# Optimization experiments

Measured on AMD Instinct MI355X. Metric: run time of the kernel, lower is better.

Reference implementation:

```python
import jax, jax.numpy as jnp
import numpy as np

HEADS = 8
DIM_HEAD = 64
SCALE = DIM_HEAD ** -0.5


def setup_inputs() -> dict:
    key = jax.random.key(0)
    ks = jax.random.split(key, 8)
    B, Nq, Nk, D = 4, 1024, 2048, 512
    inner = HEADS * DIM_HEAD  # 512
    x = jax.random.normal(ks[0], (B, Nq, D), dtype=jnp.float32)
    context = jax.random.normal(ks[1], (B, Nk, D), dtype=jnp.float32)
    bias = jax.random.normal(ks[2], (B, Nq, Nk), dtype=jnp.float32)
    s = D ** -0.5
    Wq = jax.random.normal(ks[3], (inner, D), dtype=jnp.float32) * s
    Wk = jax.random.normal(ks[4], (inner, D), dtype=jnp.float32) * s
    Wv = jax.random.normal(ks[5], (inner, D), dtype=jnp.float32) * s
    Wo = jax.random.normal(ks[6], (D, inner), dtype=jnp.float32) * s
    bo = jnp.zeros((D,), dtype=jnp.float32)
    return {"x": x, "context": context, "bias": bias,
            "Wq": Wq, "Wk": Wk, "Wv": Wv, "Wo": Wo, "bo": bo}


def reference(x, context, bias, Wq, Wk, Wv, Wo, bo):
    B, Nq, _ = x.shape
    # torch Linear: y = x @ W.T ; reshape (h d) -> b h n d
    q = (x @ Wq.T).reshape(B, Nq, HEADS, DIM_HEAD).transpose(0, 2, 1, 3)
    k = (context @ Wk.T).reshape(B, -1, HEADS, DIM_HEAD).transpose(0, 2, 1, 3)
    v = (context @ Wv.T).reshape(B, -1, HEADS, DIM_HEAD).transpose(0, 2, 1, 3)
    # explicit-score fallback path (bias supplied)
    scores = jnp.einsum('bhqd,bhkd->bhqk', q, k) * SCALE
    scores = scores + bias[:, None, :, :]  # 3D bias -> (B,1,Nq,Nk)
    attn = jax.nn.softmax(scores, axis=-1)
    out = jnp.einsum('bhqk,bhkd->bhqd', attn, v)
    out = out.transpose(0, 2, 1, 3).reshape(B, Nq, HEADS * DIM_HEAD)
    return out @ Wo.T + bo
```

## Files before the change

kernel.cpp:

```cpp
#include <hip/hip_runtime.h>

#define H 8
#define DH 64
#define NQ 1024
#define NK 2048
#define DIN 512
#define B 4
#define KSPLIT 2
#define KRANGE (NK / KSPLIT)
#define KTILES (KRANGE / 64)
#define BHNQ (B * H * NQ)

typedef __bf16 bf16;
typedef __bf16 bf16x8 __attribute__((ext_vector_type(8)));
typedef __bf16 bf16x4 __attribute__((ext_vector_type(4)));
typedef float floatx4 __attribute__((ext_vector_type(4)));

__device__ inline void gload16(const void* g, void* l) {
  __builtin_amdgcn_global_load_lds(
      (const __attribute__((address_space(1))) void*)g,
      (__attribute__((address_space(3))) void*)l, 16, 0, 0);
}

__global__ void cvt_all(const float* __restrict__ x, const float* __restrict__ ctx,
                        const float* __restrict__ wq, const float* __restrict__ wk,
                        const float* __restrict__ wv, const float* __restrict__ wo,
                        bf16* xb, bf16* cb, bf16* wqb, bf16* wkb, bf16* wvb, bf16* wob) {
  long i = ((long)blockIdx.x * 256 + threadIdx.x) * 4;
  const float* s; bf16* d; long o;
  if (i < 2097152)      { s = x;   d = xb;  o = i; }
  else if (i < 6291456) { s = ctx; d = cb;  o = i - 2097152; }
  else if (i < 6553600) { s = wq;  d = wqb; o = i - 6291456; }
  else if (i < 6815744) { s = wk;  d = wkb; o = i - 6553600; }
  else if (i < 7077888) { s = wv;  d = wvb; o = i - 6815744; }
  else                  { s = wo;  d = wob; o = i - 7077888; }
  float4 f = *(const float4*)(s + o);
  bf16x4 v = { (bf16)f.x, (bf16)f.y, (bf16)f.z, (bf16)f.w };
  *(bf16x4*)(d + o) = v;
}

__global__ __launch_bounds__(256) void gemm_qkv(
    const bf16* __restrict__ xb, const bf16* __restrict__ cb,
    const bf16* __restrict__ wqb, const bf16* __restrict__ wkb, const bf16* __restrict__ wvb,
    bf16* __restrict__ qb, bf16* __restrict__ kb, bf16* __restrict__ vtb) {
  const int which = blockIdx.z;
  if (which == 0 && blockIdx.y >= 64) return;
  const bf16* A = (which == 0) ? xb : cb;
  const bf16* W = (which == 0) ? wqb : ((which == 1) ? wkb : wvb);
  bf16* outb = (which == 0) ? qb : ((which == 1) ? kb : vtb);
  const int logT = (which == 0) ? 10 : 11;
  const float scale = (which == 0) ? 0.125f : 1.0f;
  const bool vmode = (which == 2);

  __shared__ bf16 Al[2][64 * 32];
  __shared__ bf16 Bl[2][128 * 32];
  const int t = threadIdx.x;
  const int lane = t & 63, w = t >> 6;
  const int ln = lane & 15, quad = lane >> 4;
  const int wm = (w >> 1) * 32, wn = (w & 1) * 64;
  const int rowBase = blockIdx.y * 64;
  const int colBase = blockIdx.x * 128;

  floatx4 acc[2][4] = {};
  const int rA = t >> 2, oA = (t & 3) * 8;
  const int c0 = t, c1 = t + 256;
  const int rB0 = c0 >> 2, oB0 = (c0 & 3) * 8;
  const int rB1 = c1 >> 2, oB1 = (c1 & 3) * 8;
  const bf16* Ab = A + (size_t)rowBase * DIN;
  const bf16* Wb = W + (size_t)colBase * DIN;

  gload16(Ab + (size_t)rA * DIN + oA, &Al[0][t * 8]);
  gload16(Wb + (size_t)rB0 * DIN + oB0, &Bl[0][c0 * 8]);
  gload16(Wb + (size_t)rB1 * DIN + oB1, &Bl[0][c1 * 8]);
  __syncthreads();

  for (int k0 = 0; k0 < DIN; k0 += 32) {
    const int cur = (k0 >> 5) & 1, nxt = cur ^ 1;
    if (k0 + 32 < DIN) {
      gload16(Ab + (size_t)rA * DIN + k0 + 32 + oA, &Al[nxt][t * 8]);
      gload16(Wb + (size_t)rB0 * DIN + k0 + 32 + oB0, &Bl[nxt][c0 * 8]);
      gload16(Wb + (size_t)rB1 * DIN + k0 + 32 + oB1, &Bl[nxt][c1 * 8]);
    }
    bf16x8 af[2], bfr[4];
#pragma unroll
    for (int i = 0; i < 2; i++)
      af[i] = *(const bf16x8*)&Al[cur][(wm + i * 16 + ln) * 32 + quad * 8];
#pragma unroll
    for (int j = 0; j < 4; j++)
      bfr[j] = *(const bf16x8*)&Bl[cur][(wn + j * 16 + ln) * 32 + quad * 8];
    if (!vmode) {
#pragma unroll
      for (int i = 0; i < 2; i++)
#pragma unroll
        for (int j = 0; j < 4; j++)
          acc[i][j] = __builtin_amdgcn_mfma_f32_16x16x32_bf16(af[i], bfr[j], acc[i][j], 0, 0, 0);
    } else {
#pragma unroll
      for (int i = 0; i < 2; i++)
#pragma unroll
        for (int j = 0; j < 4; j++)
          acc[i][j] = __builtin_amdgcn_mfma_f32_16x16x32_bf16(bfr[j], af[i], acc[i][j], 0, 0, 0);
    }
    __syncthreads();
  }

  const int T = 1 << logT;
#pragma unroll
  for (int i = 0; i < 2; i++)
#pragma unroll
    for (int j = 0; j < 4; j++)
#pragma unroll
      for (int r = 0; r < 4; r++) {
        if (!vmode) {
          const int m = rowBase + wm + i * 16 + quad * 4 + r;
          const int n = colBase + wn + j * 16 + ln;
          const float v = acc[i][j][r] * scale;
          const int bb = m >> logT, tok = m & (T - 1);
          const int hh = n >> 6, d = n & 63;
          outb[((((size_t)(bb * H + hh)) << logT) + tok) * DH + d] = (bf16)v;
        } else {
          const int dg = colBase + wn + j * 16 + quad * 4 + r;
          const int m = rowBase + wm + i * 16 + ln;
          const int bb = m >> logT, tok = m & (T - 1);
          const int hh = dg >> 6, d = dg & 63;
          outb[(((size_t)(bb * H + hh) * DH + d) << logT) + tok] = (bf16)acc[i][j][r];
        }
      }
}

__global__ __launch_bounds__(128) void attn_fwd(
    const bf16* __restrict__ q, const bf16* __restrict__ k,
    const bf16* __restrict__ vt, const float* __restrict__ bias,
    float* __restrict__ op0, float* __restrict__ op1, float* __restrict__ lpart) {
  __shared__ bf16 KL[64 * 64];
  __shared__ bf16 VL[64 * 64];
  __shared__ bf16 Pl[2][2][16 * 64];
  const int tid = threadIdx.x;
  const int lane = tid & 63, w = tid >> 6;
  const int ln = lane & 15, quad = lane >> 4;
  const int hh = blockIdx.y;
  const int b = blockIdx.z >> 1, ks = blockIdx.z & 1;
  const int q0 = blockIdx.x * 64;
  const int k0 = ks * KRANGE;
  const size_t bh = (size_t)b * H + hh;
  const bf16* qp = q + bh * NQ * DH;
  const bf16* kp = k + bh * NK * DH;
  const bf16* vp = vt + bh * DH * NK;
  const float* bp = bias + ((size_t)b * NQ + q0 + w * 32 + quad * 4) * NK + ln;

  bf16x8 qf[2][2];
#pragma unroll
  for (int s = 0; s < 2; s++)
#pragma unroll
    for (int kc = 0; kc < 2; kc++)
      qf[s][kc] = *(const bf16x8*)(qp + (size_t)(q0 + w * 32 + s * 16 + ln) * DH + kc * 32 + quad * 8);

  floatx4 o[2][4] = {};
  floatx4 lac[2] = {};
  const bf16x8 ones = {(bf16)1.f, (bf16)1.f, (bf16)1.f, (bf16)1.f,
                       (bf16)1.f, (bf16)1.f, (bf16)1.f, (bf16)1.f};
  constexpr float L2E = 1.44269504f;
  constexpr float OFF = 34.6246810f;

  for (int tt = 0; tt < KTILES; tt++) {
    const int nk0 = k0 + tt * 64;
#pragma unroll
    for (int s = 0; s < 4; s++) {
      const int i = s * 128 + tid;
      const int sr = i >> 3, sc = (i & 7) ^ (sr & 7);
      gload16(kp + (size_t)(nk0 + sr) * DH + sc * 8, &KL[i * 8]);
      gload16(vp + (size_t)sr * NK + nk0 + sc * 8, &VL[i * 8]);
    }
    float bc[2][4][4];
#pragma unroll
    for (int s = 0; s < 2; s++)
#pragma unroll
      for (int j = 0; j < 4; j++)
#pragma unroll
        for (int r = 0; r < 4; r++)
          bc[s][j][r] = bp[(size_t)(s * 16 + r) * NK + nk0 + j * 16];
    __syncthreads();

    floatx4 s4[2][4];
#pragma unroll
    for (int s = 0; s < 2; s++)
#pragma unroll
      for (int j = 0; j < 4; j++) {
        s4[s][j][0] = bc[s][j][0]; s4[s][j][1] = bc[s][j][1];
        s4[s][j][2] = bc[s][j][2]; s4[s][j][3] = bc[s][j][3];
      }
#pragma unroll
    for (int j = 0; j < 4; j++)
#pragma unroll
      for (int kc = 0; kc < 2; kc++) {
        const int kr = j * 16 + ln;
        bf16x8 kf = *(const bf16x8*)&KL[kr * 64 + (((kc * 4 + quad) ^ (kr & 7)) * 8)];
        s4[0][j] = __builtin_amdgcn_mfma_f32_16x16x32_bf16(qf[0][kc], kf, s4[0][j], 0, 0, 0);
        s4[1][j] = __builtin_amdgcn_mfma_f32_16x16x32_bf16(qf[1][kc], kf, s4[1][j], 0, 0, 0);
      }

#pragma unroll
    for (int s = 0; s < 2; s++)
#pragma unroll
      for (int j = 0; j < 4; j++)
#pragma unroll
        for (int r = 0; r < 4; r++)
          s4[s][j][r] = exp2f(fmaf(s4[s][j][r], L2E, -OFF));

#pragma unroll
    for (int s = 0; s < 2; s++)
#pragma unroll
      for (int j = 0; j < 4; j++)
#pragma unroll
        for (int r = 0; r < 4; r++) {
          const int m = quad * 4 + r;
          Pl[w][s][m * 64 + (((j * 2 + (ln >> 3)) ^ (m & 7)) * 8) + (ln & 7)] = (bf16)s4[s][j][r];
        }
    asm volatile("s_waitcnt lgkmcnt(0)" ::: "memory");
    bf16x8 pf[2][2];
#pragma unroll
    for (int s = 0; s < 2; s++)
#pragma unroll
      for (int kc = 0; kc < 2; kc++)
        pf[s][kc] = *(const bf16x8*)&Pl[w][s][ln * 64 + (((kc * 4 + quad) ^ (ln & 7)) * 8)];

#pragma unroll
    for (int s = 0; s < 2; s++)
#pragma unroll
      for (int kc = 0; kc < 2; kc++)
        lac[s] = __builtin_amdgcn_mfma_f32_16x16x32_bf16(pf[s][kc], ones, lac[s], 0, 0, 0);

#pragma unroll
    for (int jn = 0; jn < 4; jn++)
#pragma unroll
      for (int kc = 0; kc < 2; kc++) {
        const int vr = jn * 16 + ln;
        bf16x8 vf = *(const bf16x8*)&VL[vr * 64 + (((kc * 4 + quad) ^ (vr & 7)) * 8)];
        o[0][jn] = __builtin_amdgcn_mfma_f32_16x16x32_bf16(pf[0][kc], vf, o[0][jn], 0, 0, 0);
        o[1][jn] = __builtin_amdgcn_mfma_f32_16x16x32_bf16(pf[1][kc], vf, o[1][jn], 0, 0, 0);
      }
    __syncthreads();
  }

#pragma unroll
  for (int s = 0; s < 2; s++) {
    float* op = (ks ? op1 : op0) +
                ((size_t)b * NQ + q0 + w * 32 + s * 16 + quad * 4) * DIN + hh * 64 + ln;
#pragma unroll
    for (int jn = 0; jn < 4; jn++)
#pragma unroll
      for (int r = 0; r < 4; r++)
        op[(size_t)r * DIN + jn * 16] = o[s][jn][r];
    if (ln == 0) {
      float4 lv = {lac[s][0], lac[s][1], lac[s][2], lac[s][3]};
      *(float4*)&lpart[((size_t)ks * B * H + b * H + hh) * NQ + q0 + w * 32 + s * 16 + quad * 4] = lv;
    }
  }
}

__global__ __launch_bounds__(256) void gemm_out(
    const float* __restrict__ op0, const float* __restrict__ op1,
    const float* __restrict__ lp, const bf16* __restrict__ W,
    float* __restrict__ outf, const float* __restrict__ bo) {
  __shared__ bf16 Al[2][64 * 32];
  __shared__ bf16 Bl[2][128 * 32];
  const int t = threadIdx.x;
  const int lane = t & 63, w = t >> 6;
  const int ln = lane & 15, quad = lane >> 4;
  const int wm = (w >> 1) * 32, wn = (w & 1) * 64;
  const int rowBase = blockIdx.y * 64;
  const int colBase = blockIdx.x * 128;

  floatx4 acc[2][4] = {};
  const int rA = t >> 2, oA = (t & 3) * 8;
  const int c0 = t, c1 = t + 256;
  const int rB0 = c0 >> 2, oB0 = (c0 & 3) * 8;
  const int rB1 = c1 >> 2, oB1 = (c1 & 3) * 8;
  const int m0 = rowBase + rA;
  const bf16* Wb = W + (size_t)colBase * DIN;

  float linv0[8];
#pragma unroll
  for (int h = 0; h < 8; h++) {
    const int i0 = ((m0 >> 10) * H + h) * NQ + (m0 & 1023);
    linv0[h] = 1.0f / (lp[i0] + lp[BHNQ + i0]);
  }

#define STAGE_A(K0V, BUF)                                                      \
  {                                                                            \
    const float sA = linv0[(K0V) >> 6];                                        \
    const float* pa0 = op0 + (size_t)m0 * DIN + (K0V) + oA;                    \
    const float* pa1 = op1 + (size_t)m0 * DIN + (K0V) + oA;                    \
    float4 xa = *(const float4*)pa0, xb2 = *(const float4*)(pa0 + 4);          \
    float4 ya = *(const float4*)pa1, yb = *(const float4*)(pa1 + 4);           \
    bf16x8 v0 = {(bf16)((xa.x + ya.x) * sA), (bf16)((xa.y + ya.y) * sA),       \
                 (bf16)((xa.z + ya.z) * sA), (bf16)((xa.w + ya.w) * sA),       \
                 (bf16)((xb2.x + yb.x) * sA), (bf16)((xb2.y + yb.y) * sA),     \
                 (bf16)((xb2.z + yb.z) * sA), (bf16)((xb2.w + yb.w) * sA)};    \
    *(bf16x8*)&Al[BUF][t * 8] = v0;                                            \
  }

  STAGE_A(0, 0);
  gload16(Wb + (size_t)rB0 * DIN + oB0, &Bl[0][c0 * 8]);
  gload16(Wb + (size_t)rB1 * DIN + oB1, &Bl[0][c1 * 8]);
  __syncthreads();

#pragma unroll
  for (int kk = 0; kk < 16; kk++) {
    const int cur = kk & 1, nxt = cur ^ 1;
    if (kk < 15) {
      const int k1 = (kk + 1) * 32;
      STAGE_A(k1, nxt);
      gload16(Wb + (size_t)rB0 * DIN + k1 + oB0, &Bl[nxt][c0 * 8]);
      gload16(Wb + (size_t)rB1 * DIN + k1 + oB1, &Bl[nxt][c1 * 8]);
    }
    bf16x8 af[2], bfr[4];
#pragma unroll
    for (int i = 0; i < 2; i++)
      af[i] = *(const bf16x8*)&Al[cur][(wm + i * 16 + ln) * 32 + quad * 8];
#pragma unroll
    for (int j = 0; j < 4; j++)
      bfr[j] = *(const bf16x8*)&Bl[cur][(wn + j * 16 + ln) * 32 + quad * 8];
#pragma unroll
    for (int i = 0; i < 2; i++)
#pragma unroll
      for (int j = 0; j < 4; j++)
        acc[i][j] = __builtin_amdgcn_mfma_f32_16x16x32_bf16(af[i], bfr[j], acc[i][j], 0, 0, 0);
    __syncthreads();
  }
#undef STAGE_A

#pragma unroll
  for (int i = 0; i < 2; i++)
#pragma unroll
    for (int j = 0; j < 4; j++)
#pragma unroll
      for (int r = 0; r < 4; r++) {
        const int m = rowBase + wm + i * 16 + quad * 4 + r;
        const int n = colBase + wn + j * 16 + ln;
        outf[(size_t)m * DIN + n] = acc[i][j][r] + bo[n];
      }
}

extern "C" void kernel_launch(void* const* d_in, const int* in_sizes, int n_in,
                              void* d_out, int out_size, void* d_ws, size_t ws_size,
                              hipStream_t stream) {
  const float* x    = (const float*)d_in[0];
  const float* ctx  = (const float*)d_in[1];
  const float* bias = (const float*)d_in[2];
  const float* Wq   = (const float*)d_in[3];
  const float* Wk   = (const float*)d_in[4];
  const float* Wv   = (const float*)d_in[5];
  const float* Wo   = (const float*)d_in[6];
  const float* bo   = (const float*)d_in[7];
  float* out = (float*)d_out;

  char* p = (char*)d_ws;
  bf16* xb   = (bf16*)(p + 0);
  bf16* cb   = (bf16*)(p + 4194304);
  bf16* wqb  = (bf16*)(p + 12582912);
  bf16* wkb  = (bf16*)(p + 13107200);
  bf16* wvb  = (bf16*)(p + 13631488);
  bf16* wob  = (bf16*)(p + 14155776);
  bf16* qb   = (bf16*)(p + 14680064);
  bf16* kb   = (bf16*)(p + 18874368);
  bf16* vtb  = (bf16*)(p + 27262976);
  float* op1 = (float*)(p + 35651584);
  float* lpart = (float*)(p + 44040192);
  float* op0 = (float*)cb;

  cvt_all<<<7168, 256, 0, stream>>>(x, ctx, Wq, Wk, Wv, Wo, xb, cb, wqb, wkb, wvb, wob);
  gemm_qkv<<<dim3(4, 128, 3), 256, 0, stream>>>(xb, cb, wqb, wkb, wvb, qb, kb, vtb);
  attn_fwd<<<dim3(NQ / 64, H, B * KSPLIT), 128, 0, stream>>>(qb, kb, vtb, bias, op0, op1, lpart);
  gemm_out<<<dim3(4, 64), 256, 0, stream>>>(op0, op1, lpart, wob, out, bo);
}
```

Measured before the change: 196.6 us.

## Pre-convert bias to bf16, fuse x/ctx conversion into QKV GEMM, bf16 partials

```diff
diff --git a/kernel.cpp b/kernel.cpp
--- a/kernel.cpp
+++ b/kernel.cpp
@@ -22,30 +22,29 @@
       (__attribute__((address_space(3))) void*)l, 16, 0, 0);
 }
 
-__global__ void cvt_all(const float* __restrict__ x, const float* __restrict__ ctx,
+__global__ void cvt_all(const float* __restrict__ bias,
                         const float* __restrict__ wq, const float* __restrict__ wk,
                         const float* __restrict__ wv, const float* __restrict__ wo,
-                        bf16* xb, bf16* cb, bf16* wqb, bf16* wkb, bf16* wvb, bf16* wob) {
+                        bf16* bias16, bf16* wqb, bf16* wkb, bf16* wvb, bf16* wob) {
   long i = ((long)blockIdx.x * 256 + threadIdx.x) * 4;
   const float* s; bf16* d; long o;
-  if (i < 2097152)      { s = x;   d = xb;  o = i; }
-  else if (i < 6291456) { s = ctx; d = cb;  o = i - 2097152; }
-  else if (i < 6553600) { s = wq;  d = wqb; o = i - 6291456; }
-  else if (i < 6815744) { s = wk;  d = wkb; o = i - 6553600; }
-  else if (i < 7077888) { s = wv;  d = wvb; o = i - 6815744; }
-  else                  { s = wo;  d = wob; o = i - 7077888; }
+  if (i < 8388608)      { s = bias; d = bias16; o = i; }
+  else if (i < 8650752) { s = wq;  d = wqb; o = i - 8388608; }
+  else if (i < 8912896) { s = wk;  d = wkb; o = i - 8650752; }
+  else if (i < 9175040) { s = wv;  d = wvb; o = i - 8912896; }
+  else                  { s = wo;  d = wob; o = i - 9175040; }
   float4 f = *(const float4*)(s + o);
   bf16x4 v = { (bf16)f.x, (bf16)f.y, (bf16)f.z, (bf16)f.w };
   *(bf16x4*)(d + o) = v;
 }
 
 __global__ __launch_bounds__(256) void gemm_qkv(
-    const bf16* __restrict__ xb, const bf16* __restrict__ cb,
+    const float* __restrict__ x, const float* __restrict__ ctx,
     const bf16* __restrict__ wqb, const bf16* __restrict__ wkb, const bf16* __restrict__ wvb,
     bf16* __restrict__ qb, bf16* __restrict__ kb, bf16* __restrict__ vtb) {
   const int which = blockIdx.z;
   if (which == 0 && blockIdx.y >= 64) return;
-  const bf16* A = (which == 0) ? xb : cb;
+  const float* A32 = (which == 0) ? x : ctx;
   const bf16* W = (which == 0) ? wqb : ((which == 1) ? wkb : wvb);
   bf16* outb = (which == 0) ? qb : ((which == 1) ? kb : vtb);
   const int logT = (which == 0) ? 10 : 11;
@@ -66,20 +65,29 @@
   const int c0 = t, c1 = t + 256;
   const int rB0 = c0 >> 2, oB0 = (c0 & 3) * 8;
   const int rB1 = c1 >> 2, oB1 = (c1 & 3) * 8;
-  const bf16* Ab = A + (size_t)rowBase * DIN;
+  const float* Ab = A32 + (size_t)(rowBase + rA) * DIN + oA;
   const bf16* Wb = W + (size_t)colBase * DIN;
 
-  gload16(Ab + (size_t)rA * DIN + oA, &Al[0][t * 8]);
+  float4 la0, la1;
+  la0 = *(const float4*)(Ab + 0);
+  la1 = *(const float4*)(Ab + 4);
+  {
+    bf16x8 v = {(bf16)la0.x, (bf16)la0.y, (bf16)la0.z, (bf16)la0.w,
+                (bf16)la1.x, (bf16)la1.y, (bf16)la1.z, (bf16)la1.w};
+    *(bf16x8*)&Al[0][t * 8] = v;
+  }
   gload16(Wb + (size_t)rB0 * DIN + oB0, &Bl[0][c0 * 8]);
   gload16(Wb + (size_t)rB1 * DIN + oB1, &Bl[0][c1 * 8]);
   __syncthreads();
 
-  for (int k0 = 0; k0 < DIN; k0 += 32) {
-    const int cur = (k0 >> 5) & 1, nxt = cur ^ 1;
-    if (k0 + 32 < DIN) {
-      gload16(Ab + (size_t)rA * DIN + k0 + 32 + oA, &Al[nxt][t * 8]);
-      gload16(Wb + (size_t)rB0 * DIN + k0 + 32 + oB0, &Bl[nxt][c0 * 8]);
-      gload16(Wb + (size_t)rB1 * DIN + k0 + 32 + oB1, &Bl[nxt][c1 * 8]);
+  for (int kk = 0; kk < 16; kk++) {
+    const int cur = kk & 1, nxt = cur ^ 1;
+    const int k1 = (kk + 1) * 32;
+    if (kk < 15) {
+      la0 = *(const float4*)(Ab + k1);
+      la1 = *(const float4*)(Ab + k1 + 4);
+      gload16(Wb + (size_t)rB0 * DIN + k1 + oB0, &Bl[nxt][c0 * 8]);
+      gload16(Wb + (size_t)rB1 * DIN + k1 + oB1, &Bl[nxt][c1 * 8]);
     }
     bf16x8 af[2], bfr[4];
 #pragma unroll
@@ -100,6 +108,11 @@
 #pragma unroll
         for (int j = 0; j < 4; j++)
           acc[i][j] = __builtin_amdgcn_mfma_f32_16x16x32_bf16(bfr[j], af[i], acc[i][j], 0, 0, 0);
+    }
+    if (kk < 15) {
+      bf16x8 v = {(bf16)la0.x, (bf16)la0.y, (bf16)la0.z, (bf16)la0.w,
+                  (bf16)la1.x, (bf16)la1.y, (bf16)la1.z, (bf16)la1.w};
+      *(bf16x8*)&Al[nxt][t * 8] = v;
     }
     __syncthreads();
   }
@@ -130,10 +143,11 @@
 
 __global__ __launch_bounds__(128) void attn_fwd(
     const bf16* __restrict__ q, const bf16* __restrict__ k,
-    const bf16* __restrict__ vt, const float* __restrict__ bias,
-    float* __restrict__ op0, float* __restrict__ op1, float* __restrict__ lpart) {
+    const bf16* __restrict__ vt, const bf16* __restrict__ bias16,
+    bf16* __restrict__ op0, bf16* __restrict__ op1, float* __restrict__ lpart) {
   __shared__ bf16 KL[64 * 64];
   __shared__ bf16 VL[64 * 64];
+  __shared__ bf16 BL[64 * 64];
   __shared__ bf16 Pl[2][2][16 * 64];
   const int tid = threadIdx.x;
   const int lane = tid & 63, w = tid >> 6;
@@ -146,7 +160,7 @@
   const bf16* qp = q + bh * NQ * DH;
   const bf16* kp = k + bh * NK * DH;
   const bf16* vp = vt + bh * DH * NK;
-  const float* bp = bias + ((size_t)b * NQ + q0 + w * 32 + quad * 4) * NK + ln;
+  const bf16* bb = bias16 + ((size_t)b * NQ + q0) * NK;
 
   bf16x8 qf[2][2];
 #pragma unroll
@@ -170,25 +184,11 @@
       const int sr = i >> 3, sc = (i & 7) ^ (sr & 7);
       gload16(kp + (size_t)(nk0 + sr) * DH + sc * 8, &KL[i * 8]);
       gload16(vp + (size_t)sr * NK + nk0 + sc * 8, &VL[i * 8]);
-    }
-    float bc[2][4][4];
-#pragma unroll
-    for (int s = 0; s < 2; s++)
-#pragma unroll
-      for (int j = 0; j < 4; j++)
-#pragma unroll
-        for (int r = 0; r < 4; r++)
-          bc[s][j][r] = bp[(size_t)(s * 16 + r) * NK + nk0 + j * 16];
+      gload16(bb + (size_t)sr * NK + nk0 + sc * 8, &BL[i * 8]);
+    }
     __syncthreads();
 
-    floatx4 s4[2][4];
-#pragma unroll
-    for (int s = 0; s < 2; s++)
-#pragma unroll
-      for (int j = 0; j < 4; j++) {
-        s4[s][j][0] = bc[s][j][0]; s4[s][j][1] = bc[s][j][1];
-        s4[s][j][2] = bc[s][j][2]; s4[s][j][3] = bc[s][j][3];
-      }
+    floatx4 s4[2][4] = {};
 #pragma unroll
     for (int j = 0; j < 4; j++)
 #pragma unroll
@@ -204,8 +204,11 @@
 #pragma unroll
       for (int j = 0; j < 4; j++)
 #pragma unroll
-        for (int r = 0; r < 4; r++)
-          s4[s][j][r] = exp2f(fmaf(s4[s][j][r], L2E, -OFF));
+        for (int r = 0; r < 4; r++) {
+          const int m = w * 32 + s * 16 + quad * 4 + r;
+          const float bv = (float)BL[m * 64 + (((j * 2 + (ln >> 3)) ^ (m & 7)) * 8) + (ln & 7)];
+          s4[s][j][r] = exp2f(fmaf(s4[s][j][r] + bv, L2E, -OFF));
+        }
 
 #pragma unroll
     for (int s = 0; s < 2; s++)
@@ -244,13 +247,13 @@
 
 #pragma unroll
   for (int s = 0; s < 2; s++) {
-    float* op = (ks ? op1 : op0) +
-                ((size_t)b * NQ + q0 + w * 32 + s * 16 + quad * 4) * DIN + hh * 64 + ln;
+    bf16* op = (ks ? op1 : op0) +
+               ((size_t)b * NQ + q0 + w * 32 + s * 16 + quad * 4) * DIN + hh * 64 + ln;
 #pragma unroll
     for (int jn = 0; jn < 4; jn++)
 #pragma unroll
       for (int r = 0; r < 4; r++)
-        op[(size_t)r * DIN + jn * 16] = o[s][jn][r];
+        op[(size_t)r * DIN + jn * 16] = (bf16)o[s][jn][r];
     if (ln == 0) {
       float4 lv = {lac[s][0], lac[s][1], lac[s][2], lac[s][3]};
       *(float4*)&lpart[((size_t)ks * B * H + b * H + hh) * NQ + q0 + w * 32 + s * 16 + quad * 4] = lv;
@@ -259,7 +262,7 @@
 }
 
 __global__ __launch_bounds__(256) void gemm_out(
-    const float* __restrict__ op0, const float* __restrict__ op1,
+    const bf16* __restrict__ op0, const bf16* __restrict__ op1,
     const float* __restrict__ lp, const bf16* __restrict__ W,
     float* __restrict__ outf, const float* __restrict__ bo) {
   __shared__ bf16 Al[2][64 * 32];
@@ -289,14 +292,12 @@
 #define STAGE_A(K0V, BUF)                                                      \
   {                                                                            \
     const float sA = linv0[(K0V) >> 6];                                        \
-    const float* pa0 = op0 + (size_t)m0 * DIN + (K0V) + oA;                    \
-    const float* pa1 = op1 + (size_t)m0 * DIN + (K0V) + oA;                    \
-    float4 xa = *(const float4*)pa0, xb2 = *(const float4*)(pa0 + 4);          \
-    float4 ya = *(const float4*)pa1, yb = *(const float4*)(pa1 + 4);           \
-    bf16x8 v0 = {(bf16)((xa.x + ya.x) * sA), (bf16)((xa.y + ya.y) * sA),       \
-                 (bf16)((xa.z + ya.z) * sA), (bf16)((xa.w + ya.w) * sA),       \
-                 (bf16)((xb2.x + yb.x) * sA), (bf16)((xb2.y + yb.y) * sA),     \
-                 (bf16)((xb2.z + yb.z) * sA), (bf16)((xb2.w + yb.w) * sA)};    \
+    bf16x8 u0 = *(const bf16x8*)(op0 + (size_t)m0 * DIN + (K0V) + oA);         \
+    bf16x8 u1 = *(const bf16x8*)(op1 + (size_t)m0 * DIN + (K0V) + oA);         \
+    bf16x8 v0;                                                                 \
+    _Pragma("unroll")                                                          \
+    for (int e = 0; e < 8; e++)                                                \
+      v0[e] = (bf16)(((float)u0[e] + (float)u1[e]) * sA);                      \
     *(bf16x8*)&Al[BUF][t * 8] = v0;                                            \
   }
 
@@ -356,21 +357,20 @@
   float* out = (float*)d_out;
 
   char* p = (char*)d_ws;
-  bf16* xb   = (bf16*)(p + 0);
-  bf16* cb   = (bf16*)(p + 4194304);
-  bf16* wqb  = (bf16*)(p + 12582912);
-  bf16* wkb  = (bf16*)(p + 13107200);
-  bf16* wvb  = (bf16*)(p + 13631488);
-  bf16* wob  = (bf16*)(p + 14155776);
-  bf16* qb   = (bf16*)(p + 14680064);
-  bf16* kb   = (bf16*)(p + 18874368);
-  bf16* vtb  = (bf16*)(p + 27262976);
-  float* op1 = (float*)(p + 35651584);
-  float* lpart = (float*)(p + 44040192);
-  float* op0 = (float*)cb;
-
-  cvt_all<<<7168, 256, 0, stream>>>(x, ctx, Wq, Wk, Wv, Wo, xb, cb, wqb, wkb, wvb, wob);
-  gemm_qkv<<<dim3(4, 128, 3), 256, 0, stream>>>(xb, cb, wqb, wkb, wvb, qb, kb, vtb);
-  attn_fwd<<<dim3(NQ / 64, H, B * KSPLIT), 128, 0, stream>>>(qb, kb, vtb, bias, op0, op1, lpart);
+  bf16* bias16 = (bf16*)(p + 0);
+  bf16* wqb  = (bf16*)(p + 16777216);
+  bf16* wkb  = (bf16*)(p + 17301504);
+  bf16* wvb  = (bf16*)(p + 17825792);
+  bf16* wob  = (bf16*)(p + 18350080);
+  bf16* qb   = (bf16*)(p + 18874368);
+  bf16* kb   = (bf16*)(p + 23068672);
+  bf16* vtb  = (bf16*)(p + 31457280);
+  bf16* op0  = (bf16*)(p + 39845888);
+  bf16* op1  = (bf16*)(p + 44040192);
+  float* lpart = (float*)(p + 48234496);
+
+  cvt_all<<<9216, 256, 0, stream>>>(bias, Wq, Wk, Wv, Wo, bias16, wqb, wkb, wvb, wob);
+  gemm_qkv<<<dim3(4, 128, 3), 256, 0, stream>>>(x, ctx, wqb, wkb, wvb, qb, kb, vtb);
+  attn_fwd<<<dim3(NQ / 64, H, B * KSPLIT), 128, 0, stream>>>(qb, kb, vtb, bias16, op0, op1, lpart);
   gemm_out<<<dim3(4, 64), 256, 0, stream>>>(op0, op1, lpart, wob, out, bo);
 }
```

New measurement: 201.5 us. +2.5%, slower.
